# Optimization experiments

Measured on AMD Instinct MI355X. Metric: run time of the kernel, lower is better.

Reference implementation:

```python
import jax, jax.numpy as jnp
import numpy as np

EPS = 1e-8
B, CIN, COUT, T, H, W = 16, 16, 64, 50, 32, 32
K = 3  # cubic kernel

# Surrogate-gradient Heaviside spike: forward = step(mthr > 0),
# backward = sigma * sigmoid'(sigma * mthr) (standard SurrogateHeaviside).
@jax.custom_vjp
def spike_fn(mthr, sigma):
    return (mthr > 0.0).astype(mthr.dtype)

def _spk_fwd(mthr, sigma):
    return spike_fn(mthr, sigma), (mthr, sigma)

def _spk_bwd(res, g):
    mthr, sigma = res
    sig = jax.nn.sigmoid(sigma * mthr)
    dsig = sig * (1.0 - sig)
    return (g * sigma * dsig, jnp.sum(g * mthr * dsig).reshape(sigma.shape))

spike_fn.defvjp(_spk_fwd, _spk_bwd)


def setup_inputs() -> dict:
    key = jax.random.key(0)
    k1, k2, k3 = jax.random.split(key, 3)
    x = jax.random.normal(k1, (B, CIN, T, H, W), dtype=jnp.float32)
    # torch init: normal(mean=0, std=w_init_std*sqrt(1/(in_ch*prod(kernel))))
    w = jax.random.normal(k2, (COUT, CIN, K, K, K), jnp.float32) * np.sqrt(1.0 / (CIN * K * K * K)).astype(np.float32)
    v = jax.random.normal(k3, (COUT, COUT), jnp.float32) * np.sqrt(1.0 / COUT).astype(np.float32)
    beta = jnp.full((1,), 0.85, jnp.float32)       # one_per_layer, constant init, clamped [0,1]
    b = jnp.ones((COUT,), jnp.float32)             # constant init 1.0, clamped >= 0
    sigma = jnp.full((1,), 10.0, jnp.float32)      # surrogate_sigma, 'one' mode
    return {"x": x, "w": w, "v": v, "beta": beta, "b": b, "sigma": sigma}


def reference(x, w, v, beta, b, sigma):
    # conv3d front-end, padding=ceil((k-1)*d/2)=1, then crop to output_shape (no-op here)
    conv_x = jax.lax.conv_general_dilated(
        x, w, window_strides=(1, 1, 1), padding=[(1, 1), (1, 1), (1, 1)],
        dimension_numbers=("NCDHW", "OIDHW", "NCDHW"))
    conv_x = conv_x[:, :, :, :H, :W]  # [B, COUT, T, H, W]

    d = jnp.einsum("abcde,fbcde->af", w, w)          # [COUT, COUT] lateral reset mixing
    norm = jnp.sum(w * w, axis=(1, 2, 3, 4))          # [COUT]
    inv_norm = (1.0 / (norm + EPS))[None, :, None, None]
    bmat = b[None, :, None, None]

    batch = x.shape[0]
    mem0 = jnp.zeros((batch, COUT, H, W), x.dtype)
    spk0 = jnp.zeros_like(mem0)
    conv_seq = jnp.moveaxis(conv_x, 2, 0)             # [T, B, COUT, H, W]

    def step(carry, inp_t):
        mem, spk = carry
        rst = jnp.einsum("bchw,ce->behw", spk, d)                 # lateral reset
        inp = inp_t + jnp.einsum("bchw,ce->behw", spk, v)         # recurrent input
        mem = (mem - rst) * beta + inp * (1.0 - beta)             # leaky soft-reset LIF
        mthr = mem * inv_norm - bmat
        spk = spike_fn(mthr, sigma)
        return (mem, spk), spk

    _, spks = jax.lax.scan(step, (mem0, spk0), conv_seq)
    spk_rec = jnp.moveaxis(spks, 0, 2)                # [B, COUT, T, H, W]

    loss = 0.5 * jnp.mean(spk_rec ** 2)
    denom = jnp.asarray(batch * COUT * H * W, spk_rec.dtype)
    spk_spread_loss = jnp.max(jnp.sum(spk_rec, axis=(0, 1, 3, 4))) / denom
    return spk_rec, loss, spk_spread_loss
```

## Files before the change

kernel.cpp:

```cpp
#include <hip/hip_runtime.h>

#define NB    16
#define NCIN  16
#define NCOUT 64
#define NT    50
#define NH    32
#define NW    32
#define NHW   1024
#define WROW  432


__global__ __launch_bounds__(64) void gram_kernel(const float* __restrict__ w,
                                                  float* __restrict__ dmat,
                                                  float* __restrict__ invn) {
    const int c = blockIdx.x;
    const int e = threadIdx.x;
    const float* wc = w + c * WROW;
    const float* we = w + e * WROW;
    float acc = 0.f;
    for (int k = 0; k < WROW; ++k) acc = fmaf(wc[k], we[k], acc);
    dmat[c * 64 + e] = acc;
    if (c == e) invn[e] = 1.0f / (acc + 1e-8f);
}

__global__ __launch_bounds__(256) void wtrans_kernel(const float* __restrict__ w,
                                                     float* __restrict__ wT) {
    int idx = blockIdx.x * 256 + threadIdx.x;
    int r = idx >> 6;
    int o = idx & 63;
    wT[idx] = w[o * WROW + r];
}

#define XROW 33
#define XPLANE (34 * XROW)
#define XTOT (3 * XPLANE)

__global__ __launch_bounds__(256) void conv_kernel(const float* __restrict__ x,
                                                   const float* __restrict__ wT,
                                                   float* __restrict__ convo) {
    const int og  = blockIdx.x;
    const int t   = blockIdx.y;
    const int b   = blockIdx.z;
    const int tid = threadIdx.x;

    __shared__ float xt[2][XTOT];

    bool pv[3];
    pv[0] = (t >= 1);
    pv[1] = true;
    pv[2] = (t <= NT - 2);

    const float4* x4 = (const float4*)x;
    const long gb = ((long)b * NCIN * NT + (t - 1)) * 256 + tid;

    float4 pf[3];
#pragma unroll
    for (int kt = 0; kt < 3; ++kt)
        if (pv[kt]) pf[kt] = x4[gb + kt * 256];

    for (int i = tid; i < XTOT; i += 256) { xt[0][i] = 0.f; xt[1][i] = 0.f; }

    const int h  = tid >> 3;
    const int w0 = (tid & 7) << 2;
    const int lbase = (h + 1) * XROW + (w0 + 1);

    const float* wtg = wT + og * 8;

    float acc[8][4];
#pragma unroll
    for (int oi = 0; oi < 8; ++oi)
#pragma unroll
        for (int p = 0; p < 4; ++p) acc[oi][p] = 0.f;

    __syncthreads();

#pragma unroll
    for (int kt = 0; kt < 3; ++kt) {
        if (pv[kt]) {
            float* d = &xt[0][kt * XPLANE + lbase];
            d[0] = pf[kt].x; d[1] = pf[kt].y; d[2] = pf[kt].z; d[3] = pf[kt].w;
        }
    }
#pragma unroll
    for (int kt = 0; kt < 3; ++kt)
        if (pv[kt]) pf[kt] = x4[gb + (long)(NT * 256) + kt * 256];

    __syncthreads();

    int cur = 0;
#pragma unroll 1
    for (int c = 0; c < NCIN; ++c) {
        if (c + 1 < NCIN) {
#pragma unroll
            for (int kt = 0; kt < 3; ++kt) {
                if (pv[kt]) {
                    float* d = &xt[cur ^ 1][kt * XPLANE + lbase];
                    d[0] = pf[kt].x; d[1] = pf[kt].y; d[2] = pf[kt].z; d[3] = pf[kt].w;
                }
            }
            if (c + 2 < NCIN) {
                const long g = gb + (long)(c + 2) * (NT * 256);
#pragma unroll
                for (int kt = 0; kt < 3; ++kt)
                    if (pv[kt]) pf[kt] = x4[g + kt * 256];
            }
        }

        const float* slab = &xt[cur][0];
#pragma unroll
        for (int kt = 0; kt < 3; ++kt) {
#pragma unroll
            for (int kh = 0; kh < 3; ++kh) {
                const float* xp = &slab[kt * XPLANE + (h + kh) * XROW + w0];
                float xv[6];
#pragma unroll
                for (int j = 0; j < 6; ++j) xv[j] = xp[j];
#pragma unroll
                for (int kw = 0; kw < 3; ++kw) {
                    const float* wrow = wtg + (c * 27 + kt * 9 + kh * 3 + kw) * 64;
#pragma unroll
                    for (int oi = 0; oi < 8; ++oi) {
                        const float wv = wrow[oi];
#pragma unroll
                        for (int p = 0; p < 4; ++p)
                            acc[oi][p] = fmaf(wv, xv[kw + p], acc[oi][p]);
                    }
                }
            }
        }

        __syncthreads();
        cur ^= 1;
    }

    const size_t pxbase = ((size_t)(b * NT + t) * NHW + h * NW + w0) * NCOUT + og * 8;
#pragma unroll
    for (int p = 0; p < 4; ++p) {
        float4 v0 = make_float4(acc[0][p], acc[1][p], acc[2][p], acc[3][p]);
        float4 v1 = make_float4(acc[4][p], acc[5][p], acc[6][p], acc[7][p]);
        float4* dst = (float4*)(convo + pxbase + (size_t)p * NCOUT);
        dst[0] = v0;
        dst[1] = v1;
    }
}

__global__ __launch_bounds__(256) void scan_kernel(const float* __restrict__ convo,
                                                   const float* __restrict__ vmatg,
                                                   const float* __restrict__ betap,
                                                   const float* __restrict__ bp,
                                                   const float* __restrict__ dmatg,
                                                   const float* __restrict__ invng,
                                                   unsigned long long* __restrict__ bits) {
    const int tid  = threadIdx.x;
    const int wv   = (blockIdx.x << 2) + (tid >> 6);
    const int lane = tid & 63;
    const int b  = wv >> 10;
    const int px = wv & 1023;

    const float beta = betap[0];
    const float omb  = 1.0f - beta;
    const float bb   = bp[lane];
    const float inv  = invng[lane];

    float mem = 0.f;
    unsigned long long mask = 0ull;

    const float* cbase = convo + ((size_t)(b * NT) * NHW + px) * NCOUT + lane;
    const size_t bitbase = (size_t)(b * NT) * NHW + px;

    float cv_next = cbase[0];
    for (int t = 0; t < NT; ++t) {
        float cv = cv_next;
        if (t + 1 < NT) cv_next = cbase[(size_t)(t + 1) * NHW * NCOUT];

        float rst = 0.f, vin = 0.f;
        unsigned long long m = mask;
        while (m) {
            int c = __builtin_ctzll(m);
            m &= m - 1;
            rst += dmatg[(c << 6) + lane];
            vin += vmatg[(c << 6) + lane];
        }
        float inp = cv + vin;
        mem  = fmaf(mem - rst, beta, inp * omb);
        float mthr = fmaf(mem, inv, -bb);
        int s = mthr > 0.0f;
        mask = __ballot(s);
        if (lane == 0) bits[bitbase + (size_t)t * NHW] = mask;
    }
}

__global__ __launch_bounds__(256) void count_kernel(const unsigned long long* __restrict__ bits,
                                                    int* __restrict__ cnt) {
    const int t = blockIdx.x;
    int sum = 0;
    for (int i = threadIdx.x; i < NB * NHW; i += 256) {
        int b  = i >> 10;
        int px = i & 1023;
        sum += __popcll(bits[((size_t)(b * NT + t) << 10) + px]);
    }
    __shared__ int sh[4];
#pragma unroll
    for (int off = 32; off > 0; off >>= 1) sum += __shfl_down(sum, off);
    if ((threadIdx.x & 63) == 0) sh[threadIdx.x >> 6] = sum;
    __syncthreads();
    if (threadIdx.x == 0) cnt[t] = sh[0] + sh[1] + sh[2] + sh[3];
}

__global__ __launch_bounds__(256) void unpack_kernel(const unsigned long long* __restrict__ bits,
                                                     float* __restrict__ out) {
    const long long total4 = 13107200;
    const long long stride = (long long)gridDim.x * blockDim.x;
    for (long long i4 = (long long)blockIdx.x * 256 + threadIdx.x; i4 < total4; i4 += stride) {
        long long flat = i4 << 2;
        int hw = (int)(flat & 1023);
        long long r = flat >> 10;
        int t = (int)(r % 50);
        long long r2 = r / 50;
        int o = (int)(r2 & 63);
        int b = (int)(r2 >> 6);
        const unsigned long long* bq = bits + ((long long)(b * NT + t) << 10) + hw;
        float4 v;
        v.x = (float)((bq[0] >> o) & 1ull);
        v.y = (float)((bq[1] >> o) & 1ull);
        v.z = (float)((bq[2] >> o) & 1ull);
        v.w = (float)((bq[3] >> o) & 1ull);
        *(float4*)(out + flat) = v;
    }
}

__global__ __launch_bounds__(64) void finalize_kernel(const int* __restrict__ cnt,
                                                      float* __restrict__ out) {
    const int lane = threadIdx.x;
    int c = (lane < NT) ? cnt[lane] : 0;
    int tot = c, mx = c;
#pragma unroll
    for (int off = 32; off > 0; off >>= 1) {
        tot += __shfl_down(tot, off);
        mx = max(mx, __shfl_down(mx, off));
    }
    if (lane == 0) {
        out[52428800] = 0.5f * (float)tot / 52428800.0f;
        out[52428801] = (float)mx / 1048576.0f;
    }
}

extern "C" void kernel_launch(void* const* d_in, const int* in_sizes, int n_in,
                              void* d_out, int out_size, void* d_ws, size_t ws_size,
                              hipStream_t stream) {
    const float* x    = (const float*)d_in[0];
    const float* w    = (const float*)d_in[1];
    const float* v    = (const float*)d_in[2];
    const float* beta = (const float*)d_in[3];
    const float* b    = (const float*)d_in[4];
    float* out = (float*)d_out;

    char* ws = (char*)d_ws;
    float* convo              = (float*)(ws);
    float* dmat               = (float*)(ws + 209715200);
    float* invn               = (float*)(ws + 209715200 + 16384);
    unsigned long long* bits  = (unsigned long long*)(ws + 209731840);
    int* cnt                  = (int*)(ws + 216285440);
    float* wT                 = (float*)(ws + 216285696);

    gram_kernel<<<64, 64, 0, stream>>>(w, dmat, invn);
    wtrans_kernel<<<108, 256, 0, stream>>>(w, wT);
    conv_kernel<<<dim3(8, NT, NB), 256, 0, stream>>>(x, wT, convo);
    scan_kernel<<<4096, 256, 0, stream>>>(convo, v, beta, b, dmat, invn, bits);
    count_kernel<<<NT, 256, 0, stream>>>(bits, cnt);
    unpack_kernel<<<4096, 256, 0, stream>>>(bits, out);
    finalize_kernel<<<1, 64, 0, stream>>>(cnt, out);
}
```

Before: 551.9 us.

## Compute two output time steps per conv block to reuse loaded input planes

Each conv block now produces two consecutive time steps, staging four input time planes per channel in shared memory instead of three and accumulating into two sets of accumulators. Shared-memory staging traffic and global input reads per output drop, and the grid shrinks by half in the time dimension. The cost is double the accumulator registers (64 floats), a larger shared buffer, and a launch-bounds occupancy hint that could force register spills.

```diff
diff --git a/kernel.cpp b/kernel.cpp
--- a/kernel.cpp
+++ b/kernel.cpp
@@ -33,32 +33,34 @@
 
 #define XROW 33
 #define XPLANE (34 * XROW)
-#define XTOT (3 * XPLANE)
-
-__global__ __launch_bounds__(256) void conv_kernel(const float* __restrict__ x,
-                                                   const float* __restrict__ wT,
-                                                   float* __restrict__ convo) {
+#define XSLAB (4 * XPLANE)
+
+__global__ __launch_bounds__(256, 4) void conv_kernel(const float* __restrict__ x,
+                                                      const float* __restrict__ wT,
+                                                      float* __restrict__ convo) {
     const int og  = blockIdx.x;
-    const int t   = blockIdx.y;
+    const int tp  = blockIdx.y;
     const int b   = blockIdx.z;
     const int tid = threadIdx.x;
-
-    __shared__ float xt[2][XTOT];
-
-    bool pv[3];
-    pv[0] = (t >= 1);
-    pv[1] = true;
-    pv[2] = (t <= NT - 2);
+    const int t0  = tp << 1;
+
+    __shared__ float xt[2][XSLAB];
+
+    bool pvd[4];
+    pvd[0] = (t0 >= 1);
+    pvd[1] = true;
+    pvd[2] = true;
+    pvd[3] = (t0 + 2 <= NT - 1);
 
     const float4* x4 = (const float4*)x;
-    const long gb = ((long)b * NCIN * NT + (t - 1)) * 256 + tid;
-
-    float4 pf[3];
-#pragma unroll
-    for (int kt = 0; kt < 3; ++kt)
-        if (pv[kt]) pf[kt] = x4[gb + kt * 256];
-
-    for (int i = tid; i < XTOT; i += 256) { xt[0][i] = 0.f; xt[1][i] = 0.f; }
+    const long gb = ((long)b * NCIN * NT + (t0 - 1)) * 256 + tid;
+
+    float4 pf[4];
+#pragma unroll
+    for (int p = 0; p < 4; ++p)
+        if (pvd[p]) pf[p] = x4[gb + p * 256];
+
+    for (int i = tid; i < XSLAB; i += 256) { xt[0][i] = 0.f; xt[1][i] = 0.f; }
 
     const int h  = tid >> 3;
     const int w0 = (tid & 7) << 2;
@@ -66,24 +68,26 @@
 
     const float* wtg = wT + og * 8;
 
-    float acc[8][4];
+    float acc[8][2][4];
 #pragma unroll
     for (int oi = 0; oi < 8; ++oi)
 #pragma unroll
-        for (int p = 0; p < 4; ++p) acc[oi][p] = 0.f;
+        for (int tt = 0; tt < 2; ++tt)
+#pragma unroll
+            for (int p = 0; p < 4; ++p) acc[oi][tt][p] = 0.f;
 
     __syncthreads();
 
 #pragma unroll
-    for (int kt = 0; kt < 3; ++kt) {
-        if (pv[kt]) {
-            float* d = &xt[0][kt * XPLANE + lbase];
-            d[0] = pf[kt].x; d[1] = pf[kt].y; d[2] = pf[kt].z; d[3] = pf[kt].w;
-        }
-    }
-#pragma unroll
-    for (int kt = 0; kt < 3; ++kt)
-        if (pv[kt]) pf[kt] = x4[gb + (long)(NT * 256) + kt * 256];
+    for (int p = 0; p < 4; ++p) {
+        if (pvd[p]) {
+            float* d = &xt[0][p * XPLANE + lbase];
+            d[0] = pf[p].x; d[1] = pf[p].y; d[2] = pf[p].z; d[3] = pf[p].w;
+        }
+    }
+#pragma unroll
+    for (int p = 0; p < 4; ++p)
+        if (pvd[p]) pf[p] = x4[gb + (long)(NT + p) * 256];
 
     __syncthreads();
 
@@ -92,38 +96,54 @@
     for (int c = 0; c < NCIN; ++c) {
         if (c + 1 < NCIN) {
 #pragma unroll
-            for (int kt = 0; kt < 3; ++kt) {
-                if (pv[kt]) {
-                    float* d = &xt[cur ^ 1][kt * XPLANE + lbase];
-                    d[0] = pf[kt].x; d[1] = pf[kt].y; d[2] = pf[kt].z; d[3] = pf[kt].w;
+            for (int p = 0; p < 4; ++p) {
+                if (pvd[p]) {
+                    float* d = &xt[cur ^ 1][p * XPLANE + lbase];
+                    d[0] = pf[p].x; d[1] = pf[p].y; d[2] = pf[p].z; d[3] = pf[p].w;
                 }
             }
             if (c + 2 < NCIN) {
                 const long g = gb + (long)(c + 2) * (NT * 256);
 #pragma unroll
-                for (int kt = 0; kt < 3; ++kt)
-                    if (pv[kt]) pf[kt] = x4[g + kt * 256];
+                for (int p = 0; p < 4; ++p)
+                    if (pvd[p]) pf[p] = x4[g + p * 256];
             }
         }
 
         const float* slab = &xt[cur][0];
-#pragma unroll
-        for (int kt = 0; kt < 3; ++kt) {
+        const float* wc_ = wtg + c * 27 * 64;
+#pragma unroll
+        for (int p = 0; p < 4; ++p) {
+            float xv[3][6];
 #pragma unroll
             for (int kh = 0; kh < 3; ++kh) {
-                const float* xp = &slab[kt * XPLANE + (h + kh) * XROW + w0];
-                float xv[6];
-#pragma unroll
-                for (int j = 0; j < 6; ++j) xv[j] = xp[j];
+                const float* xp = &slab[p * XPLANE + (h + kh) * XROW + w0];
+#pragma unroll
+                for (int j = 0; j < 6; ++j) xv[kh][j] = xp[j];
+            }
+#pragma unroll
+            for (int kh = 0; kh < 3; ++kh) {
 #pragma unroll
                 for (int kw = 0; kw < 3; ++kw) {
-                    const float* wrow = wtg + (c * 27 + kt * 9 + kh * 3 + kw) * 64;
-#pragma unroll
-                    for (int oi = 0; oi < 8; ++oi) {
-                        const float wv = wrow[oi];
-#pragma unroll
-                        for (int p = 0; p < 4; ++p)
-                            acc[oi][p] = fmaf(wv, xv[kw + p], acc[oi][p]);
+                    if (p <= 2) {
+                        const float* wrow = wc_ + (p * 9 + kh * 3 + kw) * 64;
+#pragma unroll
+                        for (int oi = 0; oi < 8; ++oi) {
+                            const float wv = wrow[oi];
+#pragma unroll
+                            for (int q = 0; q < 4; ++q)
+                                acc[oi][0][q] = fmaf(wv, xv[kh][kw + q], acc[oi][0][q]);
+                        }
+                    }
+                    if (p >= 1) {
+                        const float* wrow = wc_ + ((p - 1) * 9 + kh * 3 + kw) * 64;
+#pragma unroll
+                        for (int oi = 0; oi < 8; ++oi) {
+                            const float wv = wrow[oi];
+#pragma unroll
+                            for (int q = 0; q < 4; ++q)
+                                acc[oi][1][q] = fmaf(wv, xv[kh][kw + q], acc[oi][1][q]);
+                        }
                     }
                 }
             }
@@ -133,14 +153,15 @@
         cur ^= 1;
     }
 
-    const size_t pxbase = ((size_t)(b * NT + t) * NHW + h * NW + w0) * NCOUT + og * 8;
-#pragma unroll
-    for (int p = 0; p < 4; ++p) {
-        float4 v0 = make_float4(acc[0][p], acc[1][p], acc[2][p], acc[3][p]);
-        float4 v1 = make_float4(acc[4][p], acc[5][p], acc[6][p], acc[7][p]);
-        float4* dst = (float4*)(convo + pxbase + (size_t)p * NCOUT);
-        dst[0] = v0;
-        dst[1] = v1;
+#pragma unroll
+    for (int tt = 0; tt < 2; ++tt) {
+        const size_t pxbase = ((size_t)(b * NT + t0 + tt) * NHW + h * NW + w0) * NCOUT + og * 8;
+#pragma unroll
+        for (int q = 0; q < 4; ++q) {
+            float4* dst = (float4*)(convo + pxbase + (size_t)q * NCOUT);
+            dst[0] = make_float4(acc[0][tt][q], acc[1][tt][q], acc[2][tt][q], acc[3][tt][q]);
+            dst[1] = make_float4(acc[4][tt][q], acc[5][tt][q], acc[6][tt][q], acc[7][tt][q]);
+        }
     }
 }
 
@@ -265,7 +286,7 @@
 
     gram_kernel<<<64, 64, 0, stream>>>(w, dmat, invn);
     wtrans_kernel<<<108, 256, 0, stream>>>(w, wT);
-    conv_kernel<<<dim3(8, NT, NB), 256, 0, stream>>>(x, wT, convo);
+    conv_kernel<<<dim3(8, NT / 2, NB), 256, 0, stream>>>(x, wT, convo);
     scan_kernel<<<4096, 256, 0, stream>>>(convo, v, beta, b, dmat, invn, bits);
     count_kernel<<<NT, 256, 0, stream>>>(bits, cnt);
     unpack_kernel<<<4096, 256, 0, stream>>>(bits, out);
```

Result: slower. 671.9 us (+21.8%).
